# Performance work log

Measured on AMD Instinct MI355X. Metric: run time of the kernel, lower is better.

Reference implementation:

```python
import jax, jax.numpy as jnp
import numpy as np

H = 768
F = 3072
NH = 12
EPS = 1e-5


def _layer_norm(x, g, b):
    mu = jnp.mean(x, axis=-1, keepdims=True)
    var = jnp.mean(jnp.square(x - mu), axis=-1, keepdims=True)
    return (x - mu) * jax.lax.rsqrt(var + EPS) * g + b


def setup_inputs() -> dict:
    key = jax.random.key(0)
    ks = jax.random.split(key, 16)
    s = 0.02
    d = {
        'x': jax.random.normal(ks[0], (2, 2048, H), jnp.float32),
        'Wq': jax.random.normal(ks[1], (H, H), jnp.float32) * s,
        'bq': jnp.zeros((H,), jnp.float32),
        'Wk': jax.random.normal(ks[2], (H, H), jnp.float32) * s,
        'bk': jnp.zeros((H,), jnp.float32),
        'Wv': jax.random.normal(ks[3], (H, H), jnp.float32) * s,
        'bv': jnp.zeros((H,), jnp.float32),
        'Wa1': jax.random.normal(ks[4], (H, H), jnp.float32) * s,
        'ba1': jnp.zeros((H,), jnp.float32),
        'g1': jnp.ones((H,), jnp.float32),
        'be1': jnp.zeros((H,), jnp.float32),
        'W1': jax.random.normal(ks[5], (H, F), jnp.float32) * s,
        'b1': jnp.zeros((F,), jnp.float32),
        'W2': jax.random.normal(ks[6], (F, H), jnp.float32) * s,
        'b2': jnp.zeros((H,), jnp.float32),
        'Wa2': jax.random.normal(ks[7], (H, H), jnp.float32) * s,
        'ba2': jnp.zeros((H,), jnp.float32),
        'g2': jnp.ones((H,), jnp.float32),
        'be2': jnp.zeros((H,), jnp.float32),
    }
    return d


def reference(x, Wq, bq, Wk, bk, Wv, bv, Wa1, ba1, g1, be1, W1, b1, W2, b2, Wa2, ba2, g2, be2):
    B, S, _ = x.shape
    Dh = H // NH
    # multi-head attention (naive: explicit scores + softmax)
    q = (x @ Wq + bq).reshape(B, S, NH, Dh)
    k = (x @ Wk + bk).reshape(B, S, NH, Dh)
    v = (x @ Wv + bv).reshape(B, S, NH, Dh)
    scores = jnp.einsum('bqhd,bkhd->bhqk', q, k) / jnp.sqrt(jnp.float32(Dh))
    att = jax.nn.softmax(scores, axis=-1)
    ctx = jnp.einsum('bhqk,bkhd->bqhd', att, v).reshape(B, S, H)
    # add_norm_1: Linear -> LayerNorm, then residual added AFTER LN (as in source)
    an1 = _layer_norm(ctx @ Wa1 + ba1, g1, be1) + x
    # feed-forward with exact GELU (torch nn.GELU default)
    ff = jax.nn.gelu(an1 @ W1 + b1, approximate=False) @ W2 + b2
    # add_norm_2: Linear -> LayerNorm, residual after LN
    out = _layer_norm(ff @ Wa2 + ba2, g2, be2) + an1
    return out
```

## Files before the change

kernel.cpp:

```cpp
#include <hip/hip_runtime.h>
#include <stdint.h>
#include <stddef.h>

#define HD 768
#define FF 3072
#define NHEAD 12
#define DHEAD 64
#define SEQ 2048
#define BATCH 2
#define NTOK (SEQ*BATCH)
#define SM_SCALE 0.18033688f

typedef __attribute__((ext_vector_type(8))) __bf16 bf16x8;
typedef __attribute__((ext_vector_type(4))) float f32x4;

__device__ __forceinline__ unsigned short f2bf(float f) {
  unsigned int u = __builtin_bit_cast(unsigned int, f);
  u += 0x7fffu + ((u >> 16) & 1u);
  return (unsigned short)(u >> 16);
}

__device__ __forceinline__ void gl16(const unsigned short* g, unsigned short* l) {
  __builtin_amdgcn_global_load_lds(
      (const __attribute__((address_space(1))) void*)g,
      (__attribute__((address_space(3))) void*)l,
      16, 0, 0);
}

__global__ void k_prep(const float* __restrict__ Wq, const float* __restrict__ Wk,
                       const float* __restrict__ Wv, const float* __restrict__ Wa1,
                       const float* __restrict__ W1, const float* __restrict__ W2,
                       const float* __restrict__ Wa2,
                       unsigned short* __restrict__ WqkvT, unsigned short* __restrict__ Wa1T,
                       unsigned short* __restrict__ W1T, unsigned short* __restrict__ W2T,
                       unsigned short* __restrict__ Wa2T,
                       const float* __restrict__ x, unsigned short* __restrict__ xb, int n4,
                       const float* __restrict__ bq, const float* __restrict__ bk,
                       const float* __restrict__ bv, float* __restrict__ biasqkv) {
  int t = blockIdx.x;
  int tid = threadIdx.x;
  if (t >= 7488) {
    int tb = t - 7488;
    if (tb < 9) {
      int idx = tb * 256 + tid;
      if (idx < 3*HD) {
        float v = idx < HD ? bq[idx] : idx < 2*HD ? bk[idx-HD] : bv[idx-2*HD];
        biasqkv[idx] = v;
      }
    }
    int i = tb * 256 + tid;
    int stride = 2048 * 256;
    for (; i < n4; i += stride) {
      float4 v = reinterpret_cast<const float4*>(x)[i];
      ushort4 o;
      o.x = f2bf(v.x); o.y = f2bf(v.y); o.z = f2bf(v.z); o.w = f2bf(v.w);
      reinterpret_cast<ushort4*>(xb)[i] = o;
    }
    return;
  }
  __shared__ float tile[32][33];
  const float* in; unsigned short* out; int K, N;
  if (t < 2304)      { int seg = t / 576; t -= seg * 576; K = HD; N = HD;
                       in  = seg==0 ? Wq : seg==1 ? Wk : seg==2 ? Wv : Wa1;
                       out = seg<3 ? WqkvT + seg*HD*HD : Wa1T; }
  else if (t < 4608) { t -= 2304; in = W1;  out = W1T;  K = HD; N = FF; }
  else if (t < 6912) { t -= 4608; in = W2;  out = W2T;  K = FF; N = HD; }
  else               { t -= 6912; in = Wa2; out = Wa2T; K = HD; N = HD; }
  int nt = N / 32;
  int nb = (t % nt) * 32, kb = (t / nt) * 32;
  int tx = tid & 31, ty = tid >> 5;
  for (int i = ty; i < 32; i += 8)
    tile[i][tx] = in[(size_t)(kb + i) * N + nb + tx];
  __syncthreads();
  for (int i = ty; i < 32; i += 8)
    out[(size_t)(nb + i) * K + kb + tx] = f2bf(tile[tx][i]);
}

__global__ void k_vtrans(const unsigned short* __restrict__ qkv, unsigned short* __restrict__ vt) {
  __shared__ unsigned short tile[32][33];
  int st = blockIdx.x * 32;
  int ct = blockIdx.y * 32;
  int b = blockIdx.z;
  int tx = threadIdx.x, ty = threadIdx.y;
  for (int i = ty; i < 32; i += 8)
    tile[i][tx] = qkv[(size_t)(b*SEQ + st + i) * 2304 + 2*HD + ct + tx];
  __syncthreads();
  for (int i = ty; i < 32; i += 8) {
    int vcol = ct + i;
    int p = st + tx;
    int k64 = p & 63;
    int news = (p & ~63) + ((k64 >> 2) & 3) * 16 + (k64 >> 4) * 4 + (k64 & 3);
    vt[((size_t)(b*NHEAD + (vcol >> 6)) * DHEAD + (vcol & 63)) * SEQ + news] = tile[tx][i];
  }
}


#define BN 128
#define BK 64

template<int MODE, int TBM>
__global__ __launch_bounds__(256, 3)
void k_gemm(const unsigned short* __restrict__ A, const unsigned short* __restrict__ Bt,
            const float* __restrict__ bias, void* __restrict__ Cout,
            int M, int N, int K) {
  constexpr int MR = TBM / 32;
  constexpr int AI = TBM / 32;
  __shared__ unsigned short As[TBM*BK];
  __shared__ unsigned short Bs[BN*BK];
  int tid = threadIdx.x;
  int bm = blockIdx.x * TBM;
  int bn = blockIdx.y * BN;
  int wave = tid >> 6, lane = tid & 63;
  int wm = wave >> 1, wn = wave & 1;
  int wr = wm * (TBM/2);
  int wc = wn * 64;
  int fr = lane & 15;
  int hi = lane >> 4;

  f32x4 acc[MR][4];
#pragma unroll
  for (int m = 0; m < MR; ++m)
#pragma unroll
    for (int n = 0; n < 4; ++n) acc[m][n] = (f32x4){0.f,0.f,0.f,0.f};

  int g8 = lane >> 3;
  int cc = (lane & 7) ^ g8;
  int arow = (TBM/4)*wave + g8;
  int brow = 32*wave + g8;
  const unsigned short* ag = A + (size_t)(bm + arow) * K + cc*8;
  const unsigned short* bg = Bt + (size_t)(bn + brow) * K + cc*8;
  unsigned short* asl = As + (TBM/4)*wave*BK;
  unsigned short* bsl = Bs + 32*wave*BK;

  for (int k0 = 0; k0 < K; k0 += BK) {
#pragma unroll
    for (int i = 0; i < AI; ++i)
      gl16(ag + (size_t)(8*i)*K + k0, asl + (8*i)*BK);
#pragma unroll
    for (int i = 0; i < 4; ++i)
      gl16(bg + (size_t)(8*i)*K + k0, bsl + (8*i)*BK);
    __syncthreads();

    bf16x8 af[MR][2], bf[4][2];
#pragma unroll
    for (int m = 0; m < MR; ++m) {
      int R = wr + m*16 + fr, sw = R & 7;
#pragma unroll
      for (int h2 = 0; h2 < 2; ++h2)
        af[m][h2] = __builtin_bit_cast(bf16x8,
          *reinterpret_cast<const uint4*>(&As[R*BK + ((hi + h2*4) ^ sw)*8]));
    }
#pragma unroll
    for (int n = 0; n < 4; ++n) {
      int R = wc + n*16 + fr, sw = R & 7;
#pragma unroll
      for (int h2 = 0; h2 < 2; ++h2)
        bf[n][h2] = __builtin_bit_cast(bf16x8,
          *reinterpret_cast<const uint4*>(&Bs[R*BK + ((hi + h2*4) ^ sw)*8]));
    }
#pragma unroll
    for (int m = 0; m < MR; ++m)
#pragma unroll
      for (int n = 0; n < 4; ++n) {
        acc[m][n] = __builtin_amdgcn_mfma_f32_16x16x32_bf16(af[m][0], bf[n][0], acc[m][n], 0, 0, 0);
        acc[m][n] = __builtin_amdgcn_mfma_f32_16x16x32_bf16(af[m][1], bf[n][1], acc[m][n], 0, 0, 0);
      }
    __syncthreads();
  }

  int crow0 = (lane >> 4) * 4;
  int ccol = lane & 15;
#pragma unroll
  for (int m = 0; m < MR; ++m) {
#pragma unroll
    for (int n = 0; n < 4; ++n) {
      int gcol = bn + wc + n*16 + ccol;
      float bv_ = bias[gcol];
#pragma unroll
      for (int r = 0; r < 4; ++r) {
        int grow = bm + wr + m*16 + crow0 + r;
        float v = acc[m][n][r] + bv_;
        if (MODE == 2) v = 0.5f * v * (1.0f + erff(v * 0.70710678118f));
        if (MODE == 3 && gcol < HD) v *= SM_SCALE;
        if (MODE == 0) reinterpret_cast<float*>(Cout)[(size_t)grow * N + gcol] = v;
        else           reinterpret_cast<unsigned short*>(Cout)[(size_t)grow * N + gcol] = f2bf(v);
      }
    }
  }
}


#define KVB 64
#define KP 72

__global__ __launch_bounds__(256, 3)
void k_attn_mfma(const unsigned short* __restrict__ qkv,
                 const unsigned short* __restrict__ vt,
                 unsigned short* __restrict__ ctx) {
  __shared__ unsigned short Ks[KVB][KP];
  __shared__ unsigned short Vt[DHEAD][KP];
  __shared__ f32x4 Mg[2][9][64];

  int tid = threadIdx.x;
  int wv = tid >> 6, lane = tid & 63;
  int lo = lane & 15, hi = lane >> 4;
  int qh = wv & 1;
  int kh = wv >> 1;

  int lin = blockIdx.x + 32*(blockIdx.y + NHEAD*blockIdx.z);
  int nl = (lin & 7) * 96 + (lin >> 3);
  int qb = nl & 31;
  int rest = nl >> 5;
  int h = rest % NHEAD;
  int b = rest / NHEAD;
  int q0 = qb * 64;

  const unsigned short* qpA = qkv + (size_t)(b*SEQ + q0 + qh*32 + lo) * 2304 + h*DHEAD + hi*8;
  const unsigned short* qpB = qpA + (size_t)16 * 2304;
  bf16x8 qfA0 = __builtin_bit_cast(bf16x8, *reinterpret_cast<const uint4*>(qpA));
  bf16x8 qfA1 = __builtin_bit_cast(bf16x8, *reinterpret_cast<const uint4*>(qpA + 32));
  bf16x8 qfB0 = __builtin_bit_cast(bf16x8, *reinterpret_cast<const uint4*>(qpB));
  bf16x8 qfB1 = __builtin_bit_cast(bf16x8, *reinterpret_cast<const uint4*>(qpB + 32));

  f32x4 poA[4], poB[4];
#pragma unroll
  for (int dt = 0; dt < 4; ++dt) { poA[dt] = (f32x4){0.f,0.f,0.f,0.f}; poB[dt] = (f32x4){0.f,0.f,0.f,0.f}; }
  float lrA = 0.f, lrB = 0.f;

  int sr = tid >> 2, scg = (tid & 3) * 16;
  const unsigned short* kgl = qkv + (size_t)(b*SEQ)*2304 + HD + h*DHEAD;
  const unsigned short* vgl = vt + ((size_t)(b*NHEAD + h)) * DHEAD * SEQ;

  for (int t0 = 0; t0 < SEQ; t0 += KVB) {
    const unsigned short* kp = kgl + (size_t)(t0 + sr)*2304 + scg;
    const unsigned short* vp = vgl + (size_t)sr*SEQ + t0 + scg;
    uint4 ku0 = *reinterpret_cast<const uint4*>(kp);
    uint4 ku1 = *reinterpret_cast<const uint4*>(kp + 8);
    uint4 vu0 = *reinterpret_cast<const uint4*>(vp);
    uint4 vu1 = *reinterpret_cast<const uint4*>(vp + 8);
    __syncthreads();
    *reinterpret_cast<uint4*>(&Ks[sr][scg])     = ku0;
    *reinterpret_cast<uint4*>(&Ks[sr][scg + 8]) = ku1;
    *reinterpret_cast<uint4*>(&Vt[sr][scg])     = vu0;
    *reinterpret_cast<uint4*>(&Vt[sr][scg + 8]) = vu1;
    __syncthreads();

    f32x4 sA[2], sB[2];
#pragma unroll
    for (int kg = 0; kg < 2; ++kg) {
      int krow = kh*32 + kg*16 + lo;
      bf16x8 a0 = __builtin_bit_cast(bf16x8, *reinterpret_cast<const uint4*>(&Ks[krow][hi*8]));
      bf16x8 a1 = __builtin_bit_cast(bf16x8, *reinterpret_cast<const uint4*>(&Ks[krow][32 + hi*8]));
      f32x4 s = (f32x4){0.f,0.f,0.f,0.f};
      s = __builtin_amdgcn_mfma_f32_16x16x32_bf16(a0, qfA0, s, 0, 0, 0);
      s = __builtin_amdgcn_mfma_f32_16x16x32_bf16(a1, qfA1, s, 0, 0, 0);
      sA[kg] = s;
      s = (f32x4){0.f,0.f,0.f,0.f};
      s = __builtin_amdgcn_mfma_f32_16x16x32_bf16(a0, qfB0, s, 0, 0, 0);
      s = __builtin_amdgcn_mfma_f32_16x16x32_bf16(a1, qfB1, s, 0, 0, 0);
      sB[kg] = s;
    }

    float tsA = 0.f, tsB = 0.f;
    unsigned int pwA[4], pwB[4];
#pragma unroll
    for (int kg = 0; kg < 2; ++kg) {
      float a0 = exp2f(sA[kg][0]), a1 = exp2f(sA[kg][1]);
      float a2 = exp2f(sA[kg][2]), a3 = exp2f(sA[kg][3]);
      tsA += a0 + a1 + a2 + a3;
      asm("v_cvt_pk_bf16_f32 %0, %1, %2" : "=v"(pwA[kg*2])   : "v"(a0), "v"(a1));
      asm("v_cvt_pk_bf16_f32 %0, %1, %2" : "=v"(pwA[kg*2+1]) : "v"(a2), "v"(a3));
      float b0 = exp2f(sB[kg][0]), b1 = exp2f(sB[kg][1]);
      float b2 = exp2f(sB[kg][2]), b3 = exp2f(sB[kg][3]);
      tsB += b0 + b1 + b2 + b3;
      asm("v_cvt_pk_bf16_f32 %0, %1, %2" : "=v"(pwB[kg*2])   : "v"(b0), "v"(b1));
      asm("v_cvt_pk_bf16_f32 %0, %1, %2" : "=v"(pwB[kg*2+1]) : "v"(b2), "v"(b3));
    }
    tsA += __shfl_xor(tsA, 16); tsA += __shfl_xor(tsA, 32); lrA += tsA;
    tsB += __shfl_xor(tsB, 16); tsB += __shfl_xor(tsB, 32); lrB += tsB;

    uint4 uA; uA.x = pwA[0]; uA.y = pwA[1]; uA.z = pwA[2]; uA.w = pwA[3];
    uint4 uB; uB.x = pwB[0]; uB.y = pwB[1]; uB.z = pwB[2]; uB.w = pwB[3];
    bf16x8 paA = __builtin_bit_cast(bf16x8, uA);
    bf16x8 paB = __builtin_bit_cast(bf16x8, uB);

#pragma unroll
    for (int dt = 0; dt < 4; ++dt) {
      int col = dt*16 + lo;
      bf16x8 vv = __builtin_bit_cast(bf16x8, *reinterpret_cast<const uint4*>(&Vt[col][hi*16 + kh*8]));
      poA[dt] = __builtin_amdgcn_mfma_f32_16x16x32_bf16(paA, vv, poA[dt], 0, 0, 0);
      poB[dt] = __builtin_amdgcn_mfma_f32_16x16x32_bf16(paB, vv, poB[dt], 0, 0, 0);
    }
  }

  if (kh == 1) {
#pragma unroll
    for (int dt = 0; dt < 4; ++dt) {
      Mg[qh][dt][lane] = poA[dt];
      Mg[qh][4 + dt][lane] = poB[dt];
    }
    Mg[qh][8][lane] = (f32x4){lrA, lrB, 0.f, 0.f};
  }
  __syncthreads();
  if (kh == 0) {
#pragma unroll
    for (int dt = 0; dt < 4; ++dt) {
      f32x4 mA = Mg[qh][dt][lane], mB = Mg[qh][4 + dt][lane];
      poA[dt][0] += mA[0]; poA[dt][1] += mA[1]; poA[dt][2] += mA[2]; poA[dt][3] += mA[3];
      poB[dt][0] += mB[0]; poB[dt][1] += mB[1]; poB[dt][2] += mB[2]; poB[dt][3] += mB[3];
    }
    f32x4 lm = Mg[qh][8][lane];
    lrA += lm[0]; lrB += lm[1];

    unsigned short* op = ctx + (size_t)(b*SEQ + q0 + qh*32) * HD + h*DHEAD;
#pragma unroll
    for (int r = 0; r < 4; ++r) {
      float LA = __shfl(lrA, hi*4 + r);
      float LB = __shfl(lrB, hi*4 + r);
      float liA = (LA > 0.f) ? 1.0f / LA : 0.f;
      float liB = (LB > 0.f) ? 1.0f / LB : 0.f;
      int row = hi*4 + r;
#pragma unroll
      for (int dt = 0; dt < 4; ++dt) {
        op[(size_t)row*HD + dt*16 + lo]        = f2bf(poA[dt][r] * liA);
        op[(size_t)(16 + row)*HD + dt*16 + lo] = f2bf(poB[dt][r] * liB);
      }
    }
  }
}

template<int WRITE_BF16>
__global__ __launch_bounds__(256, 4)
void k_ln(const float* __restrict__ xin, const float* __restrict__ resid,
          const float* __restrict__ g, const float* __restrict__ be,
          float* __restrict__ outf, unsigned short* __restrict__ outb) {
  int wave = threadIdx.x >> 6, lane = threadIdx.x & 63;
  int row = blockIdx.x * 4 + wave;
  const float4* xp = reinterpret_cast<const float4*>(xin + (size_t)row * HD);
  const float4* rp = reinterpret_cast<const float4*>(resid + (size_t)row * HD);
  const float4* gp = reinterpret_cast<const float4*>(g);
  const float4* bp = reinterpret_cast<const float4*>(be);
  float4 v[3];
  float sum = 0.f, sq = 0.f;
#pragma unroll
  for (int i = 0; i < 3; ++i) {
    v[i] = xp[lane + 64*i];
    sum += v[i].x + v[i].y + v[i].z + v[i].w;
    sq  += v[i].x*v[i].x + v[i].y*v[i].y + v[i].z*v[i].z + v[i].w*v[i].w;
  }
#pragma unroll
  for (int m = 1; m < 64; m <<= 1) { sum += __shfl_xor(sum, m); sq += __shfl_xor(sq, m); }
  float mean = sum * (1.0f/768.0f);
  float var = sq * (1.0f/768.0f) - mean*mean;
  float rstd = rsqrtf(var + 1e-5f);
#pragma unroll
  for (int i = 0; i < 3; ++i) {
    float4 gg = gp[lane + 64*i], bb = bp[lane + 64*i], rr = rp[lane + 64*i];
    float4 o;
    o.x = (v[i].x - mean)*rstd*gg.x + bb.x + rr.x;
    o.y = (v[i].y - mean)*rstd*gg.y + bb.y + rr.y;
    o.z = (v[i].z - mean)*rstd*gg.z + bb.z + rr.z;
    o.w = (v[i].w - mean)*rstd*gg.w + bb.w + rr.w;
    reinterpret_cast<float4*>(outf + (size_t)row * HD)[lane + 64*i] = o;
    if (WRITE_BF16) {
      ushort4 ob;
      ob.x = f2bf(o.x); ob.y = f2bf(o.y); ob.z = f2bf(o.z); ob.w = f2bf(o.w);
      reinterpret_cast<ushort4*>(outb + (size_t)row * HD)[lane + 64*i] = ob;
    }
  }
}


extern "C" void kernel_launch(void* const* d_in, const int* in_sizes, int n_in,
                              void* d_out, int out_size, void* d_ws, size_t ws_size,
                              hipStream_t stream) {
  const float* x   = (const float*)d_in[0];
  const float* Wq  = (const float*)d_in[1];
  const float* bq  = (const float*)d_in[2];
  const float* Wk  = (const float*)d_in[3];
  const float* bk  = (const float*)d_in[4];
  const float* Wv  = (const float*)d_in[5];
  const float* bv  = (const float*)d_in[6];
  const float* Wa1 = (const float*)d_in[7];
  const float* ba1 = (const float*)d_in[8];
  const float* g1  = (const float*)d_in[9];
  const float* be1 = (const float*)d_in[10];
  const float* W1  = (const float*)d_in[11];
  const float* b1  = (const float*)d_in[12];
  const float* W2  = (const float*)d_in[13];
  const float* b2  = (const float*)d_in[14];
  const float* Wa2 = (const float*)d_in[15];
  const float* ba2 = (const float*)d_in[16];
  const float* g2  = (const float*)d_in[17];
  const float* be2 = (const float*)d_in[18];

  char* ws = (char*)d_ws;
  size_t off = 0;
  auto alloc = [&](size_t bytes) -> void* {
    void* p = ws + off;
    off += (bytes + 255) & ~(size_t)255;
    return p;
  };
  unsigned short* xb    = (unsigned short*)alloc((size_t)NTOK*HD*2);
  unsigned short* WqkvT = (unsigned short*)alloc((size_t)3*HD*HD*2);
  unsigned short* Wa1T  = (unsigned short*)alloc((size_t)HD*HD*2);
  unsigned short* W1T   = (unsigned short*)alloc((size_t)FF*HD*2);
  unsigned short* W2T   = (unsigned short*)alloc((size_t)HD*FF*2);
  unsigned short* Wa2T  = (unsigned short*)alloc((size_t)HD*HD*2);
  float*          biasqkv = (float*)alloc((size_t)3*HD*4);
  unsigned short* qkvb  = (unsigned short*)alloc((size_t)NTOK*3*HD*2);
  unsigned short* vtb   = (unsigned short*)alloc((size_t)NTOK*HD*2);
  unsigned short* ctxb  = (unsigned short*)alloc((size_t)NTOK*HD*2);
  float*          a1    = (float*)alloc((size_t)NTOK*HD*4);
  float*          an1f  = (float*)alloc((size_t)NTOK*HD*4);
  unsigned short* an1b  = (unsigned short*)alloc((size_t)NTOK*HD*2);
  unsigned short* h1g   = (unsigned short*)alloc((size_t)NTOK*FF*2);
  unsigned short* f2b   = (unsigned short*)alloc((size_t)NTOK*HD*2);
  float*          a2    = (float*)alloc((size_t)NTOK*HD*4);
  (void)ws_size; (void)in_sizes; (void)n_in; (void)out_size;

  dim3 t32x8(32, 8);
  k_prep<<<9536, 256, 0, stream>>>(Wq, Wk, Wv, Wa1, W1, W2, Wa2,
                                   WqkvT, Wa1T, W1T, W2T, Wa2T,
                                   x, xb, NTOK*HD/4, bq, bk, bv, biasqkv);

  k_gemm<3,128><<<dim3(NTOK/128, 2304/BN), 256, 0, stream>>>(xb, WqkvT, biasqkv, qkvb, NTOK, 3*HD, HD);
  k_vtrans<<<dim3(SEQ/32, HD/32, BATCH), t32x8, 0, stream>>>(qkvb, vtb);
  k_attn_mfma<<<dim3(SEQ/64, NHEAD, BATCH), 256, 0, stream>>>(qkvb, vtb, ctxb);
  k_gemm<0,64><<<dim3(NTOK/64, HD/BN), 256, 0, stream>>>(ctxb, Wa1T, ba1, a1, NTOK, HD, HD);
  k_ln<1><<<NTOK/4, 256, 0, stream>>>(a1, x, g1, be1, an1f, an1b);
  k_gemm<2,128><<<dim3(NTOK/128, FF/BN), 256, 0, stream>>>(an1b, W1T, b1, h1g, NTOK, FF, HD);
  k_gemm<1,64><<<dim3(NTOK/64, HD/BN), 256, 0, stream>>>(h1g, W2T, b2, f2b, NTOK, HD, FF);
  k_gemm<0,64><<<dim3(NTOK/64, HD/BN), 256, 0, stream>>>(f2b, Wa2T, ba2, a2, NTOK, HD, HD);
  k_ln<0><<<NTOK/4, 256, 0, stream>>>(a2, an1f, g2, be2, (float*)d_out, nullptr);
}
```

Measured before the change: 198.4 us.

## Double-buffer GEMM LDS tiles and register-prefetch K/V in attention

Adds a DBUF template option to the GEMM so the next K-slice is loaded into a second LDS buffer while the current one feeds the MFMAs, which also cuts the barriers per iteration from two to one. It is enabled for the TBM=64 GEMMs. The attention kernel now issues the global loads for the next K/V tile into registers right after the current tile is stored to LDS, hiding load latency behind the QK/softmax/PV work. The cost is twice the LDS for the buffered GEMMs, which may lower occupancy, plus extra registers in attention.

Result: no change. 201.1 us (+1.4%).

```diff
diff --git a/kernel.cpp b/kernel.cpp
--- a/kernel.cpp
+++ b/kernel.cpp
@@ -98,15 +98,15 @@
 #define BN 128
 #define BK 64
 
-template<int MODE, int TBM>
+template<int MODE, int TBM, int DBUF>
 __global__ __launch_bounds__(256, 3)
 void k_gemm(const unsigned short* __restrict__ A, const unsigned short* __restrict__ Bt,
             const float* __restrict__ bias, void* __restrict__ Cout,
             int M, int N, int K) {
   constexpr int MR = TBM / 32;
   constexpr int AI = TBM / 32;
-  __shared__ unsigned short As[TBM*BK];
-  __shared__ unsigned short Bs[BN*BK];
+  __shared__ unsigned short As[(DBUF ? 2 : 1) * TBM * BK];
+  __shared__ unsigned short Bs[(DBUF ? 2 : 1) * BN * BK];
   int tid = threadIdx.x;
   int bm = blockIdx.x * TBM;
   int bn = blockIdx.y * BN;
@@ -129,18 +129,21 @@
   int brow = 32*wave + g8;
   const unsigned short* ag = A + (size_t)(bm + arow) * K + cc*8;
   const unsigned short* bg = Bt + (size_t)(bn + brow) * K + cc*8;
-  unsigned short* asl = As + (TBM/4)*wave*BK;
-  unsigned short* bsl = Bs + 32*wave*BK;
-
-  for (int k0 = 0; k0 < K; k0 += BK) {
+
+  auto stage = [&](int buf, int k0) {
+    unsigned short* asd = As + buf*TBM*BK + (TBM/4)*wave*BK;
+    unsigned short* bsd = Bs + buf*BN*BK + 32*wave*BK;
 #pragma unroll
     for (int i = 0; i < AI; ++i)
-      gl16(ag + (size_t)(8*i)*K + k0, asl + (8*i)*BK);
+      gl16(ag + (size_t)(8*i)*K + k0, asd + (8*i)*BK);
 #pragma unroll
     for (int i = 0; i < 4; ++i)
-      gl16(bg + (size_t)(8*i)*K + k0, bsl + (8*i)*BK);
-    __syncthreads();
-
+      gl16(bg + (size_t)(8*i)*K + k0, bsd + (8*i)*BK);
+  };
+
+  auto compute = [&](int buf) {
+    const unsigned short* Asb = As + buf*TBM*BK;
+    const unsigned short* Bsb = Bs + buf*BN*BK;
     bf16x8 af[MR][2], bf[4][2];
 #pragma unroll
     for (int m = 0; m < MR; ++m) {
@@ -148,7 +151,7 @@
 #pragma unroll
       for (int h2 = 0; h2 < 2; ++h2)
         af[m][h2] = __builtin_bit_cast(bf16x8,
-          *reinterpret_cast<const uint4*>(&As[R*BK + ((hi + h2*4) ^ sw)*8]));
+          *reinterpret_cast<const uint4*>(&Asb[R*BK + ((hi + h2*4) ^ sw)*8]));
     }
 #pragma unroll
     for (int n = 0; n < 4; ++n) {
@@ -156,7 +159,7 @@
 #pragma unroll
       for (int h2 = 0; h2 < 2; ++h2)
         bf[n][h2] = __builtin_bit_cast(bf16x8,
-          *reinterpret_cast<const uint4*>(&Bs[R*BK + ((hi + h2*4) ^ sw)*8]));
+          *reinterpret_cast<const uint4*>(&Bsb[R*BK + ((hi + h2*4) ^ sw)*8]));
     }
 #pragma unroll
     for (int m = 0; m < MR; ++m)
@@ -165,7 +168,24 @@
         acc[m][n] = __builtin_amdgcn_mfma_f32_16x16x32_bf16(af[m][0], bf[n][0], acc[m][n], 0, 0, 0);
         acc[m][n] = __builtin_amdgcn_mfma_f32_16x16x32_bf16(af[m][1], bf[n][1], acc[m][n], 0, 0, 0);
       }
-    __syncthreads();
+  };
+
+  if (DBUF) {
+    stage(0, 0);
+    int cur = 0;
+    for (int k0 = 0; k0 < K; k0 += BK) {
+      __syncthreads();
+      if (k0 + BK < K) stage(cur ^ 1, k0 + BK);
+      compute(cur);
+      cur ^= 1;
+    }
+  } else {
+    for (int k0 = 0; k0 < K; k0 += BK) {
+      stage(0, k0);
+      __syncthreads();
+      compute(0);
+      __syncthreads();
+    }
   }
 
   int crow0 = (lane >> 4) * 4;
@@ -231,19 +251,32 @@
   const unsigned short* kgl = qkv + (size_t)(b*SEQ)*2304 + HD + h*DHEAD;
   const unsigned short* vgl = vt + ((size_t)(b*NHEAD + h)) * DHEAD * SEQ;
 
+  uint4 ku0, ku1, vu0, vu1;
+  {
+    const unsigned short* kp = kgl + (size_t)sr*2304 + scg;
+    const unsigned short* vp = vgl + (size_t)sr*SEQ + scg;
+    ku0 = *reinterpret_cast<const uint4*>(kp);
+    ku1 = *reinterpret_cast<const uint4*>(kp + 8);
+    vu0 = *reinterpret_cast<const uint4*>(vp);
+    vu1 = *reinterpret_cast<const uint4*>(vp + 8);
+  }
+
   for (int t0 = 0; t0 < SEQ; t0 += KVB) {
-    const unsigned short* kp = kgl + (size_t)(t0 + sr)*2304 + scg;
-    const unsigned short* vp = vgl + (size_t)sr*SEQ + t0 + scg;
-    uint4 ku0 = *reinterpret_cast<const uint4*>(kp);
-    uint4 ku1 = *reinterpret_cast<const uint4*>(kp + 8);
-    uint4 vu0 = *reinterpret_cast<const uint4*>(vp);
-    uint4 vu1 = *reinterpret_cast<const uint4*>(vp + 8);
     __syncthreads();
     *reinterpret_cast<uint4*>(&Ks[sr][scg])     = ku0;
     *reinterpret_cast<uint4*>(&Ks[sr][scg + 8]) = ku1;
     *reinterpret_cast<uint4*>(&Vt[sr][scg])     = vu0;
     *reinterpret_cast<uint4*>(&Vt[sr][scg + 8]) = vu1;
     __syncthreads();
+
+    if (t0 + KVB < SEQ) {
+      const unsigned short* kp = kgl + (size_t)(t0 + KVB + sr)*2304 + scg;
+      const unsigned short* vp = vgl + (size_t)sr*SEQ + (t0 + KVB) + scg;
+      ku0 = *reinterpret_cast<const uint4*>(kp);
+      ku1 = *reinterpret_cast<const uint4*>(kp + 8);
+      vu0 = *reinterpret_cast<const uint4*>(vp);
+      vu1 = *reinterpret_cast<const uint4*>(vp + 8);
+    }
 
     f32x4 sA[2], sB[2];
 #pragma unroll
@@ -424,13 +457,13 @@
                                    WqkvT, Wa1T, W1T, W2T, Wa2T,
                                    x, xb, NTOK*HD/4, bq, bk, bv, biasqkv);
 
-  k_gemm<3,128><<<dim3(NTOK/128, 2304/BN), 256, 0, stream>>>(xb, WqkvT, biasqkv, qkvb, NTOK, 3*HD, HD);
+  k_gemm<3,128,0><<<dim3(NTOK/128, 2304/BN), 256, 0, stream>>>(xb, WqkvT, biasqkv, qkvb, NTOK, 3*HD, HD);
   k_vtrans<<<dim3(SEQ/32, HD/32, BATCH), t32x8, 0, stream>>>(qkvb, vtb);
   k_attn_mfma<<<dim3(SEQ/64, NHEAD, BATCH), 256, 0, stream>>>(qkvb, vtb, ctxb);
-  k_gemm<0,64><<<dim3(NTOK/64, HD/BN), 256, 0, stream>>>(ctxb, Wa1T, ba1, a1, NTOK, HD, HD);
+  k_gemm<0,64,1><<<dim3(NTOK/64, HD/BN), 256, 0, stream>>>(ctxb, Wa1T, ba1, a1, NTOK, HD, HD);
   k_ln<1><<<NTOK/4, 256, 0, stream>>>(a1, x, g1, be1, an1f, an1b);
-  k_gemm<2,128><<<dim3(NTOK/128, FF/BN), 256, 0, stream>>>(an1b, W1T, b1, h1g, NTOK, FF, HD);
-  k_gemm<1,64><<<dim3(NTOK/64, HD/BN), 256, 0, stream>>>(h1g, W2T, b2, f2b, NTOK, HD, FF);
-  k_gemm<0,64><<<dim3(NTOK/64, HD/BN), 256, 0, stream>>>(f2b, Wa2T, ba2, a2, NTOK, HD, HD);
+  k_gemm<2,128,0><<<dim3(NTOK/128, FF/BN), 256, 0, stream>>>(an1b, W1T, b1, h1g, NTOK, FF, HD);
+  k_gemm<1,64,1><<<dim3(NTOK/64, HD/BN), 256, 0, stream>>>(h1g, W2T, b2, f2b, NTOK, HD, FF);
+  k_gemm<0,64,1><<<dim3(NTOK/64, HD/BN), 256, 0, stream>>>(f2b, Wa2T, ba2, a2, NTOK, HD, HD);
   k_ln<0><<<NTOK/4, 256, 0, stream>>>(a2, an1f, g2, be2, (float*)d_out, nullptr);
 }
```
